# Kernel optimization log

Hardware: AMD Instinct MI355X
Metric: run time of the kernel (lower is better)

Reference implementation:

```python
import jax, jax.numpy as jnp
import numpy as np
jax.config.update("jax_enable_x64", True)  # faithful int64 spatial hashing as in torch

T = 524288            # hash table size per level
NL = jnp.asarray([16, 22, 30, 42, 58, 80, 110, 152, 209, 288, 397, 547, 754, 1039, 1432, 1974], dtype=jnp.float32)
L = 16
SCALE = 3.0
L_EMBED = 4
PI2 = 2654435761
PI3 = 805459861
NPTS = 524288

_k = np.arange(8)
# ceil/floor selector per original vertex enumeration, axis order (x, y, z)
CEIL_BITS = jnp.asarray(np.stack([
    [0, 1, 0, 0, 0, 1, 1, 1],   # x uses ceil
    [0, 0, 1, 0, 1, 0, 1, 1],   # y uses ceil
    [0, 0, 0, 1, 1, 1, 0, 1],   # z uses ceil
], axis=-1).astype(bool))        # [8,3]
# grid_sample places vertex k at grid (d,h,w)=(k//4,(k//2)%2,k%2); with align_corners=False
# on a 2x2x2 grid and grid coord frac-0.5, the weight for index 1 along W/H/D is frac_x/frac_y/frac_z.
# (This faithfully reproduces the original's vertex/weight mismatch.)
WEIGHT_BITS = jnp.asarray(np.stack([_k % 2, (_k // 2) % 2, _k // 4], axis=-1).astype(bool))  # [8,3]


def hash_features(xu, tables):
    # xu: [N,3] in ~[0,1]; tables: [L,T,2]
    def level(_, xs):
        n, table = xs
        p = xu * n
        pf = jnp.floor(p)
        pc = jnp.ceil(p)
        frac = p - pf                                                        # [N,3]
        verts = jnp.where(CEIL_BITS[None], pc[:, None, :], pf[:, None, :]).astype(jnp.int64)  # [N,8,3]
        h = ((verts[..., 0] * 1) ^ (verts[..., 1] * PI2) ^ (verts[..., 2] * PI3)) % T          # [N,8]
        w = jnp.prod(jnp.where(WEIGHT_BITS[None], frac[:, None, :], 1.0 - frac[:, None, :]), axis=-1)  # [N,8]
        feat = jnp.einsum('nk,nkf->nf', w.astype(table.dtype), table[h])    # [N,2]
        return None, feat
    _, feats = jax.lax.scan(level, None, (NL, tables))                       # [L,N,2]
    return jnp.transpose(feats, (1, 0, 2)).reshape(xu.shape[0], -1)          # [N,2L]


def posenc(d):
    outs = [d]
    for i in range(L_EMBED):
        s = (2.0 ** i) * d
        outs.append(jnp.sin(s))
        outs.append(jnp.cos(s))
    return jnp.concatenate(outs, -1)  # [N, 3+6*L_EMBED]


def setup_inputs() -> dict:
    key = jax.random.key(0)
    ks = jax.random.split(key, 16)
    f32 = jnp.float32
    s = 0.05
    return {
        "x": jax.random.normal(ks[0], (NPTS, 3), f32),
        "d": jax.random.normal(ks[1], (NPTS, 3), f32),
        "tables": (jax.random.uniform(ks[2], (L, T, 2), f32) * 2.0 - 1.0) * 1e-4,
        "w1a": jax.random.normal(ks[3], (2 * L, 64), f32) * s,
        "b1a": jnp.zeros((64,), f32),
        "w1b": jax.random.normal(ks[4], (64, 16), f32) * s,
        "b1b": jnp.zeros((16,), f32),
        "w2a": jax.random.normal(ks[5], (16 + 3 + 6 * L_EMBED, 64), f32) * s,
        "b2a": jnp.zeros((64,), f32),
        "w2b": jax.random.normal(ks[6], (64, 64), f32) * s,
        "b2b": jnp.zeros((64,), f32),
        "w2c": jax.random.normal(ks[7], (64, 3), f32) * s,
        "b2c": jnp.zeros((3,), f32),
    }


def reference(x, d, tables, w1a, b1a, w1b, b1b, w2a, b2a, w2b, b2b, w2c, b2c):
    xs = x / SCALE
    mask = (jnp.abs(xs[:, 0]) < 0.5) & (jnp.abs(xs[:, 1]) < 0.5) & (jnp.abs(xs[:, 2]) < 0.5)
    xu = xs + 0.5
    feats = hash_features(xu, tables)                     # [N, 32]
    h = jax.nn.relu(feats @ w1a + b1a) @ w1b + b1b        # [N, 16]
    log_sigma = jnp.where(mask, h[:, 0], -100000.0)
    z = jnp.concatenate([h, posenc(d)], -1)               # [N, 43]
    z = jax.nn.relu(z @ w2a + b2a)
    z = jax.nn.relu(z @ w2b + b2b)
    c = jax.nn.sigmoid(z @ w2c + b2c)
    color = jnp.where(mask[:, None], c, 0.0)
    return color, jnp.exp(log_sigma)
```

## Files before the change

kernel.cpp:

```cpp
#include <hip/hip_runtime.h>
#include <math.h>

#define NPTS 524288
#define HALF (NPTS / 2)
#define TSZ  524288
#define TMASK (TSZ - 1)
#define FP8SCALE 4096.0f
#define FP8INV   (1.0f / 4096.0f)

typedef __attribute__((ext_vector_type(8))) short v8s;
typedef __attribute__((ext_vector_type(4))) float v4f;
typedef __attribute__((ext_vector_type(2))) float v2f;

#define MFMA16(a, b, c) __builtin_amdgcn_mfma_f32_16x16x32_bf16(a, b, c, 0, 0, 0)

__device__ __constant__ float NLf[16] = {
    16.f, 22.f, 30.f, 42.f, 58.f, 80.f, 110.f, 152.f,
    209.f, 288.f, 397.f, 547.f, 754.f, 1039.f, 1432.f, 1974.f
};

#define CEILX 0xE2
#define CEILY 0xD4
#define CEILZ 0xB8

__device__ __forceinline__ short bf16r(float v) {
    unsigned b = __float_as_uint(v);
    b += 0x7FFFu + ((b >> 16) & 1u);
    return (short)(b >> 16);
}
__device__ __forceinline__ unsigned packbf(float a, float b) {
    return (unsigned)(unsigned short)bf16r(a) | ((unsigned)(unsigned short)bf16r(b) << 16);
}
__device__ __forceinline__ unsigned sel4(uint4 t, unsigned i) {
    const unsigned ab = (i & 1u) ? t.y : t.x;
    const unsigned cd = (i & 1u) ? t.w : t.z;
    return (i & 2u) ? cd : ab;
}
__device__ __forceinline__ unsigned sel8(uint4 t, unsigned i) {
    const unsigned w = sel4(t, i >> 1);
    return (i & 1u) ? (w >> 16) : (w & 0xFFFFu);
}

__global__ __launch_bounds__(256) void pack_tables(
    const float4* __restrict__ tbl, unsigned* __restrict__ out,
    unsigned* __restrict__ idxbuf, unsigned* __restrict__ cnt)
{
    const int idx = blockIdx.x * 256 + threadIdx.x;
    const float4 t = tbl[idx];
    const unsigned lo = (unsigned)__builtin_amdgcn_cvt_pk_fp8_f32(
                            t.x * FP8SCALE, t.y * FP8SCALE, 0, false) & 0xFFFFu;
    const unsigned hi = (unsigned)__builtin_amdgcn_cvt_pk_fp8_f32(
                            t.z * FP8SCALE, t.w * FP8SCALE, 0, false) & 0xFFFFu;
    out[idx] = lo | (hi << 16);
    if (idx < NPTS) idxbuf[idx] = 0xFFFFFFFFu;
    if (idx == 0) cnt[0] = 0u;
}

#define W1A_OFF 0
#define W1B_OFF 2560
#define W2A_OFF 3712
#define W2B_OFF 8320
#define W2C_OFF 12928
#define WPK_TOT 14080

__global__ __launch_bounds__(1024) void ngp_packw(
    const float* __restrict__ w1a, const float* __restrict__ w1b,
    const float* __restrict__ w2a, const float* __restrict__ w2b,
    const float* __restrict__ w2c, unsigned short* __restrict__ wpk)
{
    const int s = blockIdx.x * 1024 + threadIdx.x;
    if (s >= WPK_TOT) return;
    float v = 0.f;
    if (s < W1B_OFF) {
        const int r = s - W1A_OFF, n = r / 40, k = r % 40;
        v = (k < 32) ? w1a[k * 64 + n] : 0.f;
    } else if (s < W2A_OFF) {
        const int r = s - W1B_OFF, n = r / 72, k = r % 72;
        v = (k < 64) ? w1b[k * 16 + n] : 0.f;
    } else if (s < W2B_OFF) {
        const int r = s - W2A_OFF, n = r / 72, k = r % 72;
        v = (k < 43) ? w2a[k * 64 + n] : 0.f;
    } else if (s < W2C_OFF) {
        const int r = s - W2B_OFF, n = r / 72, k = r % 72;
        v = (k < 64) ? w2b[k * 64 + n] : 0.f;
    } else {
        const int r = s - W2C_OFF, n = r / 72, k = r % 72;
        v = (k < 64 && n < 3) ? w2c[k * 3 + n] : 0.f;
    }
    wpk[s] = (unsigned short)bf16r(v);
}

__global__ __launch_bounds__(1024) void ngp_compact2(
    const float* __restrict__ x, const float* __restrict__ d,
    unsigned* __restrict__ idxbuf, float* __restrict__ xc,
    float* __restrict__ dc, unsigned* __restrict__ cnt,
    float* __restrict__ out)
{
    __shared__ unsigned sWCnt[16];
    __shared__ unsigned sBase;

    const int tid  = threadIdx.x;
    const int wv   = tid >> 6, lane = tid & 63;
    const int i    = blockIdx.x * 1024 + tid;

    const float x0 = x[3*i+0], x1 = x[3*i+1], x2 = x[3*i+2];
    const float xs0 = x0 / 3.0f, xs1 = x1 / 3.0f, xs2 = x2 / 3.0f;
    const bool act = (fabsf(xs0) < 0.5f) && (fabsf(xs1) < 0.5f) && (fabsf(xs2) < 0.5f);
    if (!act) {
        out[3*i+0] = 0.f; out[3*i+1] = 0.f; out[3*i+2] = 0.f;
        out[3*NPTS + i] = 0.f;
    }
    const unsigned long long mb = __ballot(act);
    if (lane == 0) sWCnt[wv] = (unsigned)__popcll(mb);
    __syncthreads();
    if (tid == 0) {
        unsigned tot = 0;
        #pragma unroll
        for (int w = 0; w < 16; ++w) tot += sWCnt[w];
        sBase = atomicAdd(cnt, tot);
    }
    __syncthreads();
    if (act) {
        unsigned off = sBase;
        for (int w = 0; w < wv; ++w) off += sWCnt[w];
        off += (unsigned)__popcll(mb & ((1ull << lane) - 1ull));
        idxbuf[off] = (unsigned)i;
        xc[3*off+0] = x0; xc[3*off+1] = x1; xc[3*off+2] = x2;
        dc[3*off+0] = d[3*i+0]; dc[3*off+1] = d[3*i+1]; dc[3*off+2] = d[3*i+2];
    }
}

__global__ __launch_bounds__(256) void ngp_hash6(
    const float* __restrict__ xc, const unsigned short* __restrict__ tables_pk,
    const unsigned* __restrict__ cnt, unsigned* __restrict__ feats_pk)
{
    __shared__ float sX[768];
    const int NC = (int)cnt[0];
    if (blockIdx.x * 256 >= NC) return;

    const int tid = threadIdx.x;
    const int l = blockIdx.y;
    const float n = NLf[l];
    const unsigned short* tbl = tables_pk + (size_t)l * TSZ;

    for (int r = tid; r < 768; r += 256)
        sX[r] = xc[(size_t)blockIdx.x * 768 + r];
    __syncthreads();

    const int j = blockIdx.x * 256 + tid;
    const float xu0 = sX[tid * 3 + 0] / 3.0f + 0.5f;
    const float xu1 = sX[tid * 3 + 1] / 3.0f + 0.5f;
    const float xu2 = sX[tid * 3 + 2] / 3.0f + 0.5f;

    const float p0 = xu0 * n, p1 = xu1 * n, p2 = xu2 * n;
    const float f0 = floorf(p0), f1 = floorf(p1), f2 = floorf(p2);
    const float fr0 = p0 - f0, fr1 = p1 - f1, fr2 = p2 - f2;
    const float g0 = 1.f - fr0, g1 = 1.f - fr1, g2 = 1.f - fr2;
    const unsigned uvf0 = (unsigned)(int)f0;
    const unsigned uvc0 = (unsigned)(int)ceilf(p0);
    const unsigned syf = (unsigned)(int)f1 * 2654435761u;
    const unsigned syc = (unsigned)(int)ceilf(p1) * 2654435761u;
    const unsigned szf = (unsigned)(int)f2 * 805459861u;
    const unsigned szc = (unsigned)(int)ceilf(p2) * 805459861u;

    const float w0 = g0 * g1 * g2,  w1 = fr0 * g1 * g2;
    const float w2 = g0 * fr1 * g2, w6 = g0 * fr1 * fr2;
    const float w3 = fr0 * fr1 * g2, w5 = fr0 * g1 * fr2;
    const float w4 = g0 * g1 * fr2, w7 = fr0 * fr1 * fr2;

    const unsigned Ss[4] = { syf ^ szf, syc ^ szf, syf ^ szc, syc ^ szc };
    const float wf[4] = { w0, w2, w3, w4 };
    const float wc[4] = { w1, w6, w5, w7 };

    float a0 = 0.f, a1 = 0.f;
    #pragma unroll
    for (int pr = 0; pr < 4; ++pr) {
        const unsigned hf = (Ss[pr] ^ uvf0) & TMASK;
        const unsigned hc = (Ss[pr] ^ uvc0) & TMASK;
        const unsigned diff = hf ^ hc;
        const uint4 tv = *(const uint4*)(tbl + (hf & ~7u));
        const unsigned ef = sel8(tv, hf & 7u);
        unsigned ec;
        if (diff <= 7u) ec = sel8(tv, hc & 7u);
        else            ec = (unsigned)tbl[hc];
        const v2f ff = __builtin_amdgcn_cvt_pk_f32_fp8((int)ef, false);
        const v2f fc = __builtin_amdgcn_cvt_pk_f32_fp8((int)ec, false);
        a0 = fmaf(wf[pr], ff.x, a0);
        a1 = fmaf(wf[pr], ff.y, a1);
        a0 = fmaf(wc[pr], fc.x, a0);
        a1 = fmaf(wc[pr], fc.y, a1);
    }
    a0 *= FP8INV;
    a1 *= FP8INV;
    feats_pk[(size_t)l * NPTS + j] = packbf(a0, a1);
}

#define PZ 72
#define SWL(row) ((((row) >> 2) & 3) << 4)

__global__ __launch_bounds__(512) void ngp_mlp6(
    const float* __restrict__ dc,
    const unsigned* __restrict__ feats_pk, const unsigned* __restrict__ idxbuf,
    const unsigned* __restrict__ cnt, const unsigned short* __restrict__ wpk,
    const float* __restrict__ b1a, const float* __restrict__ b1b,
    const float* __restrict__ b2a, const float* __restrict__ b2b,
    const float* __restrict__ b2c,
    float* __restrict__ out)
{
    __shared__ short sW[WPK_TOT];
    __shared__ short sZ[8 * 16 * PZ];

    const int NC = (int)cnt[0];
    if (blockIdx.x * 512 >= NC) return;

    const int tid = threadIdx.x;
    for (int i = tid; i < WPK_TOT / 8; i += 512)
        ((uint4*)sW)[i] = ((const uint4*)wpk)[i];
    __syncthreads();

    const short* sW1a = sW + W1A_OFF;
    const short* sW1b = sW + W1B_OFF;
    const short* sW2a = sW + W2A_OFF;
    const short* sW2b = sW + W2B_OFF;
    const short* sW2c = sW + W2C_OFF;

    const int wave = tid >> 6, lane = tid & 63;
    const int m = lane & 15, q = lane >> 4;
    short* zb = &sZ[wave * 16 * PZ];

    float bb1a[4], bb2a[4], bb2b[4];
    #pragma unroll
    for (int ct = 0; ct < 4; ++ct) {
        bb1a[ct] = b1a[ct * 16 + m];
        bb2a[ct] = b2a[ct * 16 + m];
        bb2b[ct] = b2b[ct * 16 + m];
    }
    const float bb1b = b1b[m];
    const float bb2c = (m < 3) ? b2c[m] : 0.f;

    const int base = (blockIdx.x * 8 + wave) * 64;

    for (int t = 0; t < 4; ++t) {
        const int j0 = base + t * 16;
        if (j0 >= NC) break;

        #pragma unroll
        for (int it = 0; it < 4; ++it) {
            const int l = it * 4 + q;
            *(unsigned*)(zb + m * PZ + ((2 * l) ^ SWL(m))) =
                feats_pk[(size_t)l * NPTS + j0 + m];
        }

        {
            const v8s a0 = *(const v8s*)(zb + m * PZ + ((q * 8) ^ SWL(m)));
            #pragma unroll
            for (int ct = 0; ct < 4; ++ct) {
                const float bv = bb1a[ct];
                v4f acc = {bv, bv, bv, bv};
                acc = MFMA16(a0, *(const v8s*)(sW1a + (ct * 16 + m) * 40 + q * 8), acc);
                #pragma unroll
                for (int r = 0; r < 4; ++r)
                    zb[(q * 4 + r) * PZ + ((ct * 16 + m) ^ (q << 4))] = bf16r(fmaxf(acc[r], 0.f));
            }
        }

        v4f hacc;
        {
            const v8s a10 = *(const v8s*)(zb + m * PZ + ((q * 8) ^ SWL(m)));
            const v8s a11 = *(const v8s*)(zb + m * PZ + ((32 + q * 8) ^ SWL(m)));
            v4f hv = {bb1b, bb1b, bb1b, bb1b};
            hv = MFMA16(a10, *(const v8s*)(sW1b + m * 72 + q * 8), hv);
            hv = MFMA16(a11, *(const v8s*)(sW1b + m * 72 + 32 + q * 8), hv);
            hacc = hv;
            #pragma unroll
            for (int r = 0; r < 4; ++r)
                zb[(q * 4 + r) * PZ + (m ^ (q << 4))] = bf16r(hv[r]);
        }

        {
            const float dd0 = dc[3*(j0+m)+0], dd1 = dc[3*(j0+m)+1], dd2 = dc[3*(j0+m)+2];
            v8s pk;
            #pragma unroll
            for (int jj = 0; jj < 8; ++jj) {
                const int k = 16 + q * 8 + jj;
                float v;
                if (k < 19) {
                    v = (k == 16) ? dd0 : ((k == 17) ? dd1 : dd2);
                } else if (k < 43) {
                    const int idx = k - 19;
                    const int e = idx / 6, w = idx - 6 * e;
                    const float base2 = (w == 0 || w == 3) ? dd0 : ((w == 1 || w == 4) ? dd1 : dd2);
                    const float s = (float)(1 << e) * base2;
                    v = (w < 3) ? __sinf(s) : __cosf(s);
                } else {
                    v = 0.f;
                }
                pk[jj] = bf16r(v);
            }
            *(v8s*)(zb + m * PZ + ((16 + q * 8) ^ SWL(m))) = pk;
            *(unsigned long long*)(zb + m * PZ + ((48 + q * 4) ^ SWL(m))) = 0ull;
        }

        {
            const v8s a20 = *(const v8s*)(zb + m * PZ + ((q * 8) ^ SWL(m)));
            const v8s a21 = *(const v8s*)(zb + m * PZ + ((32 + q * 8) ^ SWL(m)));
            #pragma unroll
            for (int ct = 0; ct < 4; ++ct) {
                const float bv = bb2a[ct];
                v4f acc = {bv, bv, bv, bv};
                acc = MFMA16(a20, *(const v8s*)(sW2a + (ct * 16 + m) * 72 + q * 8), acc);
                acc = MFMA16(a21, *(const v8s*)(sW2a + (ct * 16 + m) * 72 + 32 + q * 8), acc);
                #pragma unroll
                for (int r = 0; r < 4; ++r)
                    zb[(q * 4 + r) * PZ + ((ct * 16 + m) ^ (q << 4))] = bf16r(fmaxf(acc[r], 0.f));
            }
        }

        {
            const v8s a20 = *(const v8s*)(zb + m * PZ + ((q * 8) ^ SWL(m)));
            const v8s a21 = *(const v8s*)(zb + m * PZ + ((32 + q * 8) ^ SWL(m)));
            #pragma unroll
            for (int ct = 0; ct < 4; ++ct) {
                const float bv = bb2b[ct];
                v4f acc = {bv, bv, bv, bv};
                acc = MFMA16(a20, *(const v8s*)(sW2b + (ct * 16 + m) * 72 + q * 8), acc);
                acc = MFMA16(a21, *(const v8s*)(sW2b + (ct * 16 + m) * 72 + 32 + q * 8), acc);
                #pragma unroll
                for (int r = 0; r < 4; ++r)
                    zb[(q * 4 + r) * PZ + ((ct * 16 + m) ^ (q << 4))] = bf16r(fmaxf(acc[r], 0.f));
            }
        }

        {
            const v8s a30 = *(const v8s*)(zb + m * PZ + ((q * 8) ^ SWL(m)));
            const v8s a31 = *(const v8s*)(zb + m * PZ + ((32 + q * 8) ^ SWL(m)));
            v4f cacc = {bb2c, bb2c, bb2c, bb2c};
            cacc = MFMA16(a30, *(const v8s*)(sW2c + m * 72 + q * 8), cacc);
            cacc = MFMA16(a31, *(const v8s*)(sW2c + m * 72 + 32 + q * 8), cacc);

            if (m < 3) {
                #pragma unroll
                for (int r = 0; r < 4; ++r) {
                    const unsigned pj = idxbuf[j0 + q * 4 + r];
                    if (pj < (unsigned)NPTS) {
                        const float cv = 1.0f / (1.0f + __expf(-cacc[r]));
                        out[3 * pj + m] = cv;
                    }
                }
            }
            if (m == 0) {
                #pragma unroll
                for (int r = 0; r < 4; ++r) {
                    const unsigned pj = idxbuf[j0 + q * 4 + r];
                    if (pj < (unsigned)NPTS)
                        out[3 * NPTS + pj] = __expf(hacc[r]);
                }
            }
        }
    }
}

__global__ __launch_bounds__(256) void ngp_fused(
    const float* __restrict__ x, const float* __restrict__ d,
    const float* __restrict__ tables,
    const float* __restrict__ w1a, const float* __restrict__ b1a,
    const float* __restrict__ w1b, const float* __restrict__ b1b,
    const float* __restrict__ w2a, const float* __restrict__ b2a,
    const float* __restrict__ w2b, const float* __restrict__ b2b,
    const float* __restrict__ w2c, const float* __restrict__ b2c,
    float* __restrict__ out)
{
    const int i = blockIdx.x * 256 + threadIdx.x;
    if (i >= NPTS) return;
    const float xs0 = x[3*i+0] / 3.0f;
    const float xs1 = x[3*i+1] / 3.0f;
    const float xs2 = x[3*i+2] / 3.0f;
    const bool mask = (fabsf(xs0) < 0.5f) & (fabsf(xs1) < 0.5f) & (fabsf(xs2) < 0.5f);
    const float xu0 = xs0 + 0.5f, xu1 = xs1 + 0.5f, xu2 = xs2 + 0.5f;

    float feats[32];
    #pragma unroll
    for (int l = 0; l < 16; ++l) {
        const float n = NLf[l];
        const float p0 = xu0 * n, p1 = xu1 * n, p2 = xu2 * n;
        const float f0 = floorf(p0), f1 = floorf(p1), f2 = floorf(p2);
        const float fr0 = p0 - f0, fr1 = p1 - f1, fr2 = p2 - f2;
        const int vf0 = (int)f0, vf1 = (int)f1, vf2 = (int)f2;
        const int vc0 = (int)ceilf(p0), vc1 = (int)ceilf(p1), vc2 = (int)ceilf(p2);
        const float2* tbl = (const float2*)(tables + (size_t)l * (TSZ * 2));
        float a0 = 0.f, a1 = 0.f;
        #pragma unroll
        for (int k = 0; k < 8; ++k) {
            const unsigned vx = (unsigned)(((CEILX >> k) & 1) ? vc0 : vf0);
            const unsigned vy = (unsigned)(((CEILY >> k) & 1) ? vc1 : vf1);
            const unsigned vz = (unsigned)(((CEILZ >> k) & 1) ? vc2 : vf2);
            const unsigned h = (vx ^ (vy * 2654435761u) ^ (vz * 805459861u)) & TMASK;
            const float wx = (k & 1)        ? fr0 : 1.0f - fr0;
            const float wy = ((k >> 1) & 1) ? fr1 : 1.0f - fr1;
            const float wz = ((k >> 2) & 1) ? fr2 : 1.0f - fr2;
            const float wgt = wx * wy * wz;
            const float2 t = tbl[h];
            a0 = fmaf(wgt, t.x, a0);
            a1 = fmaf(wgt, t.y, a1);
        }
        feats[2*l] = a0; feats[2*l+1] = a1;
    }

    float h2v[16];
    #pragma unroll
    for (int j = 0; j < 16; ++j) h2v[j] = b1b[j];
    #pragma unroll
    for (int c = 0; c < 4; ++c) {
        float h1c[16];
        #pragma unroll
        for (int jj = 0; jj < 16; ++jj) h1c[jj] = b1a[16*c + jj];
        #pragma unroll
        for (int i2 = 0; i2 < 32; ++i2) {
            const float f = feats[i2];
            #pragma unroll
            for (int jj = 0; jj < 16; ++jj)
                h1c[jj] = fmaf(f, w1a[i2*64 + 16*c + jj], h1c[jj]);
        }
        #pragma unroll
        for (int jj = 0; jj < 16; ++jj) {
            const float f = fmaxf(h1c[jj], 0.f);
            #pragma unroll
            for (int t = 0; t < 16; ++t)
                h2v[t] = fmaf(f, w1b[(16*c + jj)*16 + t], h2v[t]);
        }
    }

    float z1[64];
    #pragma unroll
    for (int j = 0; j < 64; ++j) z1[j] = b2a[j];
    #pragma unroll
    for (int i2 = 0; i2 < 16; ++i2) {
        const float f = h2v[i2];
        #pragma unroll
        for (int j = 0; j < 64; ++j) z1[j] = fmaf(f, w2a[i2*64 + j], z1[j]);
    }
    const float d0 = d[3*i+0], d1 = d[3*i+1], d2 = d[3*i+2];
    {
        const float* r = w2a + 16*64;
        #pragma unroll
        for (int j = 0; j < 64; ++j) z1[j] = fmaf(d0, r[j], z1[j]);
        r = w2a + 17*64;
        #pragma unroll
        for (int j = 0; j < 64; ++j) z1[j] = fmaf(d1, r[j], z1[j]);
        r = w2a + 18*64;
        #pragma unroll
        for (int j = 0; j < 64; ++j) z1[j] = fmaf(d2, r[j], z1[j]);
    }
    #pragma unroll
    for (int e = 0; e < 4; ++e) {
        const float mm = (float)(1 << e);
        const float dv[3] = {d0, d1, d2};
        #pragma unroll
        for (int a = 0; a < 3; ++a) {
            const float sv = __sinf(mm * dv[a]);
            const float* rs = w2a + (19 + 6*e + a)*64;
            #pragma unroll
            for (int j = 0; j < 64; ++j) z1[j] = fmaf(sv, rs[j], z1[j]);
        }
        #pragma unroll
        for (int a = 0; a < 3; ++a) {
            const float cv = __cosf(mm * dv[a]);
            const float* rc = w2a + (19 + 6*e + 3 + a)*64;
            #pragma unroll
            for (int j = 0; j < 64; ++j) z1[j] = fmaf(cv, rc[j], z1[j]);
        }
    }
    #pragma unroll
    for (int j = 0; j < 64; ++j) z1[j] = fmaxf(z1[j], 0.f);

    float ca = b2c[0], cb = b2c[1], cc = b2c[2];
    #pragma unroll
    for (int jc = 0; jc < 64; jc += 16) {
        float acc[16];
        #pragma unroll
        for (int jj = 0; jj < 16; ++jj) acc[jj] = b2b[jc + jj];
        #pragma unroll
        for (int i2 = 0; i2 < 64; ++i2) {
            const float f = z1[i2];
            #pragma unroll
            for (int jj = 0; jj < 16; ++jj)
                acc[jj] = fmaf(f, w2b[i2*64 + jc + jj], acc[jj]);
        }
        #pragma unroll
        for (int jj = 0; jj < 16; ++jj) {
            const float v = fmaxf(acc[jj], 0.f);
            ca = fmaf(v, w2c[(jc + jj)*3 + 0], ca);
            cb = fmaf(v, w2c[(jc + jj)*3 + 1], cb);
            cc = fmaf(v, w2c[(jc + jj)*3 + 2], cc);
        }
    }

    float r = 1.0f / (1.0f + __expf(-ca));
    float g = 1.0f / (1.0f + __expf(-cb));
    float b = 1.0f / (1.0f + __expf(-cc));
    float sigma;
    if (mask) { sigma = __expf(h2v[0]); }
    else { r = 0.f; g = 0.f; b = 0.f; sigma = 0.f; }
    out[3*i + 0] = r;
    out[3*i + 1] = g;
    out[3*i + 2] = b;
    out[3*NPTS + i] = sigma;
}

extern "C" void kernel_launch(void* const* d_in, const int* in_sizes, int n_in,
                              void* d_out, int out_size, void* d_ws, size_t ws_size,
                              hipStream_t stream) {
    const float* x      = (const float*)d_in[0];
    const float* d      = (const float*)d_in[1];
    const float* tables = (const float*)d_in[2];
    const float* w1a    = (const float*)d_in[3];
    const float* b1a    = (const float*)d_in[4];
    const float* w1b    = (const float*)d_in[5];
    const float* b1b    = (const float*)d_in[6];
    const float* w2a    = (const float*)d_in[7];
    const float* b2a    = (const float*)d_in[8];
    const float* w2b    = (const float*)d_in[9];
    const float* b2b    = (const float*)d_in[10];
    const float* w2c    = (const float*)d_in[11];
    const float* b2c    = (const float*)d_in[12];
    float* out = (float*)d_out;

    const size_t need = (size_t)33 * NPTS * 4;
    if (ws_size >= need) {
        unsigned* base      = (unsigned*)d_ws;
        unsigned* feats_pk  = base;
        unsigned* tables_pk = base + (size_t)16 * NPTS;
        unsigned* idxbuf    = base + (size_t)24 * NPTS;
        unsigned* cnt       = base + (size_t)25 * NPTS;
        float*    xc        = (float*)(base + (size_t)26 * NPTS);
        float*    dc        = (float*)(base + (size_t)29 * NPTS);
        unsigned short* wpk = (unsigned short*)(base + (size_t)32 * NPTS);

        dim3 gp(16 * TSZ / (256 * 2)), bp(256);
        hipLaunchKernelGGL(pack_tables, gp, bp, 0, stream,
                           (const float4*)tables, tables_pk, idxbuf, cnt);

        dim3 gw((WPK_TOT + 1023) / 1024), bw(1024);
        hipLaunchKernelGGL(ngp_packw, gw, bw, 0, stream,
                           w1a, w1b, w2a, w2b, w2c, wpk);

        dim3 gc(NPTS / 1024), bc(1024);
        hipLaunchKernelGGL(ngp_compact2, gc, bc, 0, stream,
                           x, d, idxbuf, xc, dc, cnt, out);

        dim3 gh(NPTS / 256, 16), bh(256);
        hipLaunchKernelGGL(ngp_hash6, gh, bh, 0, stream,
                           xc, (const unsigned short*)tables_pk, cnt, feats_pk);

        dim3 gm(NPTS / 512), bm(512);
        hipLaunchKernelGGL(ngp_mlp6, gm, bm, 0, stream,
                           dc, feats_pk, idxbuf, cnt, wpk,
                           b1a, b1b, b2a, b2b, b2c, out);
    } else {
        dim3 grid(NPTS / 256), block(256);
        hipLaunchKernelGGL(ngp_fused, grid, block, 0, stream,
                           x, d, tables, w1a, b1a, w1b, b1b,
                           w2a, b2a, w2b, b2b, w2c, b2c, out);
    }
}
```

Before: 265.1 us.

## Transpose MLP MFMA operands so outputs are point-major and store packed bf16 rows

Swaps the A and B operands of every MFMA so each lane holds four consecutive output features for one point. Activations can then be written back to LDS as contiguous packed uint2/uint4 stores using the hardware v_cvt_pk_bf16_f32 instruction, replacing scalar 16-bit stores with software rounding and dropping the XOR swizzle. Biases become per-lane vector loads, and the sigma/color writes become one lane per point. The unswizzled LDS layout may bring back bank conflicts, and the hardware conversion may round slightly differently from the old manual rounding.

```diff
diff --git a/kernel.cpp b/kernel.cpp
--- a/kernel.cpp
+++ b/kernel.cpp
@@ -30,6 +30,11 @@
 }
 __device__ __forceinline__ unsigned packbf(float a, float b) {
     return (unsigned)(unsigned short)bf16r(a) | ((unsigned)(unsigned short)bf16r(b) << 16);
+}
+__device__ __forceinline__ unsigned cvtpk(float a, float b) {
+    unsigned r;
+    asm("v_cvt_pk_bf16_f32 %0, %1, %2" : "=v"(r) : "v"(a), "v"(b));
+    return r;
 }
 __device__ __forceinline__ unsigned sel4(uint4 t, unsigned i) {
     const unsigned ab = (i & 1u) ? t.y : t.x;
@@ -196,9 +201,8 @@
 }
 
 #define PZ 72
-#define SWL(row) ((((row) >> 2) & 3) << 4)
-
-__global__ __launch_bounds__(512) void ngp_mlp6(
+
+__global__ __launch_bounds__(512) void ngp_mlp7(
     const float* __restrict__ dc,
     const unsigned* __restrict__ feats_pk, const unsigned* __restrict__ idxbuf,
     const unsigned* __restrict__ cnt, const unsigned short* __restrict__ wpk,
@@ -228,15 +232,16 @@
     const int m = lane & 15, q = lane >> 4;
     short* zb = &sZ[wave * 16 * PZ];
 
-    float bb1a[4], bb2a[4], bb2b[4];
+    v4f bb1a[4], bb2a[4], bb2b[4];
     #pragma unroll
     for (int ct = 0; ct < 4; ++ct) {
-        bb1a[ct] = b1a[ct * 16 + m];
-        bb2a[ct] = b2a[ct * 16 + m];
-        bb2b[ct] = b2b[ct * 16 + m];
-    }
-    const float bb1b = b1b[m];
-    const float bb2c = (m < 3) ? b2c[m] : 0.f;
+        bb1a[ct] = *(const v4f*)(b1a + ct * 16 + q * 4);
+        bb2a[ct] = *(const v4f*)(b2a + ct * 16 + q * 4);
+        bb2b[ct] = *(const v4f*)(b2b + ct * 16 + q * 4);
+    }
+    const v4f bb1b4 = *(const v4f*)(b1b + q * 4);
+    v4f bb2c4 = {0.f, 0.f, 0.f, 0.f};
+    if (q == 0) { bb2c4[0] = b2c[0]; bb2c4[1] = b2c[1]; bb2c4[2] = b2c[2]; }
 
     const int base = (blockIdx.x * 8 + wave) * 64;
 
@@ -247,39 +252,41 @@
         #pragma unroll
         for (int it = 0; it < 4; ++it) {
             const int l = it * 4 + q;
-            *(unsigned*)(zb + m * PZ + ((2 * l) ^ SWL(m))) =
+            *(unsigned*)(zb + m * PZ + 2 * l) =
                 feats_pk[(size_t)l * NPTS + j0 + m];
         }
 
         {
-            const v8s a0 = *(const v8s*)(zb + m * PZ + ((q * 8) ^ SWL(m)));
+            const v8s z0 = *(const v8s*)(zb + m * PZ + q * 8);
             #pragma unroll
             for (int ct = 0; ct < 4; ++ct) {
-                const float bv = bb1a[ct];
-                v4f acc = {bv, bv, bv, bv};
-                acc = MFMA16(a0, *(const v8s*)(sW1a + (ct * 16 + m) * 40 + q * 8), acc);
-                #pragma unroll
-                for (int r = 0; r < 4; ++r)
-                    zb[(q * 4 + r) * PZ + ((ct * 16 + m) ^ (q << 4))] = bf16r(fmaxf(acc[r], 0.f));
+                v4f acc = bb1a[ct];
+                acc = MFMA16(*(const v8s*)(sW1a + (ct * 16 + m) * 40 + q * 8), z0, acc);
+                const unsigned lo = cvtpk(fmaxf(acc[0], 0.f), fmaxf(acc[1], 0.f));
+                const unsigned hi = cvtpk(fmaxf(acc[2], 0.f), fmaxf(acc[3], 0.f));
+                *(uint2*)(zb + m * PZ + ct * 16 + q * 4) = make_uint2(lo, hi);
             }
         }
 
-        v4f hacc;
         {
-            const v8s a10 = *(const v8s*)(zb + m * PZ + ((q * 8) ^ SWL(m)));
-            const v8s a11 = *(const v8s*)(zb + m * PZ + ((32 + q * 8) ^ SWL(m)));
-            v4f hv = {bb1b, bb1b, bb1b, bb1b};
-            hv = MFMA16(a10, *(const v8s*)(sW1b + m * 72 + q * 8), hv);
-            hv = MFMA16(a11, *(const v8s*)(sW1b + m * 72 + 32 + q * 8), hv);
-            hacc = hv;
-            #pragma unroll
-            for (int r = 0; r < 4; ++r)
-                zb[(q * 4 + r) * PZ + (m ^ (q << 4))] = bf16r(hv[r]);
+            const v8s z0 = *(const v8s*)(zb + m * PZ + q * 8);
+            const v8s z1 = *(const v8s*)(zb + m * PZ + 32 + q * 8);
+            v4f hv = bb1b4;
+            hv = MFMA16(*(const v8s*)(sW1b + m * 72 + q * 8), z0, hv);
+            hv = MFMA16(*(const v8s*)(sW1b + m * 72 + 32 + q * 8), z1, hv);
+            if (q == 0) {
+                const unsigned pj = idxbuf[j0 + m];
+                if (pj < (unsigned)NPTS)
+                    out[3 * NPTS + pj] = __expf(hv[0]);
+            }
+            const unsigned lo = cvtpk(hv[0], hv[1]);
+            const unsigned hi = cvtpk(hv[2], hv[3]);
+            *(uint2*)(zb + m * PZ + q * 4) = make_uint2(lo, hi);
         }
 
         {
             const float dd0 = dc[3*(j0+m)+0], dd1 = dc[3*(j0+m)+1], dd2 = dc[3*(j0+m)+2];
-            v8s pk;
+            float pv[8];
             #pragma unroll
             for (int jj = 0; jj < 8; ++jj) {
                 const int k = 16 + q * 8 + jj;
@@ -295,65 +302,55 @@
                 } else {
                     v = 0.f;
                 }
-                pk[jj] = bf16r(v);
+                pv[jj] = v;
             }
-            *(v8s*)(zb + m * PZ + ((16 + q * 8) ^ SWL(m))) = pk;
-            *(unsigned long long*)(zb + m * PZ + ((48 + q * 4) ^ SWL(m))) = 0ull;
+            const uint4 pk4 = make_uint4(cvtpk(pv[0], pv[1]), cvtpk(pv[2], pv[3]),
+                                         cvtpk(pv[4], pv[5]), cvtpk(pv[6], pv[7]));
+            *(uint4*)(zb + m * PZ + 16 + q * 8) = pk4;
+            *(unsigned long long*)(zb + m * PZ + 48 + q * 4) = 0ull;
         }
 
         {
-            const v8s a20 = *(const v8s*)(zb + m * PZ + ((q * 8) ^ SWL(m)));
-            const v8s a21 = *(const v8s*)(zb + m * PZ + ((32 + q * 8) ^ SWL(m)));
+            const v8s z0 = *(const v8s*)(zb + m * PZ + q * 8);
+            const v8s z1 = *(const v8s*)(zb + m * PZ + 32 + q * 8);
             #pragma unroll
             for (int ct = 0; ct < 4; ++ct) {
-                const float bv = bb2a[ct];
-                v4f acc = {bv, bv, bv, bv};
-                acc = MFMA16(a20, *(const v8s*)(sW2a + (ct * 16 + m) * 72 + q * 8), acc);
-                acc = MFMA16(a21, *(const v8s*)(sW2a + (ct * 16 + m) * 72 + 32 + q * 8), acc);
-                #pragma unroll
-                for (int r = 0; r < 4; ++r)
-                    zb[(q * 4 + r) * PZ + ((ct * 16 + m) ^ (q << 4))] = bf16r(fmaxf(acc[r], 0.f));
+                v4f acc = bb2a[ct];
+                acc = MFMA16(*(const v8s*)(sW2a + (ct * 16 + m) * 72 + q * 8), z0, acc);
+                acc = MFMA16(*(const v8s*)(sW2a + (ct * 16 + m) * 72 + 32 + q * 8), z1, acc);
+                const unsigned lo = cvtpk(fmaxf(acc[0], 0.f), fmaxf(acc[1], 0.f));
+                const unsigned hi = cvtpk(fmaxf(acc[2], 0.f), fmaxf(acc[3], 0.f));
+                *(uint2*)(zb + m * PZ + ct * 16 + q * 4) = make_uint2(lo, hi);
             }
         }
 
         {
-            const v8s a20 = *(const v8s*)(zb + m * PZ + ((q * 8) ^ SWL(m)));
-            const v8s a21 = *(const v8s*)(zb + m * PZ + ((32 + q * 8) ^ SWL(m)));
+            const v8s z0 = *(const v8s*)(zb + m * PZ + q * 8);
+            const v8s z1 = *(const v8s*)(zb + m * PZ + 32 + q * 8);
             #pragma unroll
             for (int ct = 0; ct < 4; ++ct) {
-                const float bv = bb2b[ct];
-                v4f acc = {bv, bv, bv, bv};
-                acc = MFMA16(a20, *(const v8s*)(sW2b + (ct * 16 + m) * 72 + q * 8), acc);
-                acc = MFMA16(a21, *(const v8s*)(sW2b + (ct * 16 + m) * 72 + 32 + q * 8), acc);
-                #pragma unroll
-                for (int r = 0; r < 4; ++r)
-                    zb[(q * 4 + r) * PZ + ((ct * 16 + m) ^ (q << 4))] = bf16r(fmaxf(acc[r], 0.f));
+                v4f acc = bb2b[ct];
+                acc = MFMA16(*(const v8s*)(sW2b + (ct * 16 + m) * 72 + q * 8), z0, acc);
+                acc = MFMA16(*(const v8s*)(sW2b + (ct * 16 + m) * 72 + 32 + q * 8), z1, acc);
+                const unsigned lo = cvtpk(fmaxf(acc[0], 0.f), fmaxf(acc[1], 0.f));
+                const unsigned hi = cvtpk(fmaxf(acc[2], 0.f), fmaxf(acc[3], 0.f));
+                *(uint2*)(zb + m * PZ + ct * 16 + q * 4) = make_uint2(lo, hi);
             }
         }
 
         {
-            const v8s a30 = *(const v8s*)(zb + m * PZ + ((q * 8) ^ SWL(m)));
-            const v8s a31 = *(const v8s*)(zb + m * PZ + ((32 + q * 8) ^ SWL(m)));
-            v4f cacc = {bb2c, bb2c, bb2c, bb2c};
-            cacc = MFMA16(a30, *(const v8s*)(sW2c + m * 72 + q * 8), cacc);
-            cacc = MFMA16(a31, *(const v8s*)(sW2c + m * 72 + 32 + q * 8), cacc);
-
-            if (m < 3) {
-                #pragma unroll
-                for (int r = 0; r < 4; ++r) {
-                    const unsigned pj = idxbuf[j0 + q * 4 + r];
-                    if (pj < (unsigned)NPTS) {
-                        const float cv = 1.0f / (1.0f + __expf(-cacc[r]));
-                        out[3 * pj + m] = cv;
-                    }
-                }
-            }
-            if (m == 0) {
-                #pragma unroll
-                for (int r = 0; r < 4; ++r) {
-                    const unsigned pj = idxbuf[j0 + q * 4 + r];
-                    if (pj < (unsigned)NPTS)
-                        out[3 * NPTS + pj] = __expf(hacc[r]);
+            const v8s z0 = *(const v8s*)(zb + m * PZ + q * 8);
+            const v8s z1 = *(const v8s*)(zb + m * PZ + 32 + q * 8);
+            v4f cacc = bb2c4;
+            cacc = MFMA16(*(const v8s*)(sW2c + m * 72 + q * 8), z0, cacc);
+            cacc = MFMA16(*(const v8s*)(sW2c + m * 72 + 32 + q * 8), z1, cacc);
+
+            if (q == 0) {
+                const unsigned pj = idxbuf[j0 + m];
+                if (pj < (unsigned)NPTS) {
+                    out[3 * pj + 0] = 1.0f / (1.0f + __expf(-cacc[0]));
+                    out[3 * pj + 1] = 1.0f / (1.0f + __expf(-cacc[1]));
+                    out[3 * pj + 2] = 1.0f / (1.0f + __expf(-cacc[2]));
                 }
             }
         }
@@ -553,7 +550,7 @@
                            xc, (const unsigned short*)tables_pk, cnt, feats_pk);
 
         dim3 gm(NPTS / 512), bm(512);
-        hipLaunchKernelGGL(ngp_mlp6, gm, bm, 0, stream,
+        hipLaunchKernelGGL(ngp_mlp7, gm, bm, 0, stream,
                            dc, feats_pk, idxbuf, cnt, wpk,
                            b1a, b1b, b2a, b2b, b2c, out);
     } else {
```

New measurement: 255.1 us. 3.7% less time.
